# Kernel optimization log

Measured on AMD Instinct MI355X. Metric: run time of the kernel, lower is better.

The kernel has to match this reference:

```python
import jax, jax.numpy as jnp
import numpy as np

N, F, K, E = 65536, 256, 8, 2097152  # nodes, feat dim, experts, edges (avg degree 32)


def setup_inputs() -> dict:
    key = jax.random.key(0)
    ks = jax.random.split(key, 7)
    x = jax.random.normal(ks[0], (N, F), dtype=jnp.float32)
    h0 = jax.random.normal(ks[1], (N, F), dtype=jnp.float32)
    z = jax.random.uniform(ks[2], (N, K), dtype=jnp.float32)
    rows = jax.random.randint(ks[3], (E,), 0, N, dtype=jnp.int32)
    cols = jax.random.randint(ks[4], (E,), 0, N, dtype=jnp.int32)
    # normalized-ish edge weights (like sym-normalized adjacency values)
    vals = jax.random.uniform(ks[5], (E,), dtype=jnp.float32) / 32.0
    stdv = 1.0 / np.sqrt(F)  # reset_parameters: uniform(-stdv, stdv), stdv = 1/sqrt(out)
    weights = jax.random.uniform(ks[6], (K, F, F), minval=-stdv, maxval=stdv, dtype=jnp.float32)
    return {"x": x, "h0": h0, "z": z, "vals": vals, "weights": weights,
            "rows": rows, "cols": cols}


def reference(x, h0, z, vals, weights, rows, cols):
    # hi = spmm(adj, x): irregular gather + segment-sum over edge list
    hi = jax.ops.segment_sum(vals[:, None] * x[cols], rows, num_segments=N)  # [N,F]
    # variant=False: support = hi. Fused K-expert combine:
    # torch: outputs[k] = support @ W[k]; out = sum_k z[:,k,None] * outputs[k]
    out = jnp.einsum('ni,kio,nk->no', hi, weights, z)  # [N,F]
    # residual=True
    return out + x
```

## Files before the change

### kernel.cpp

```cpp
#include <hip/hip_runtime.h>
#include <hip/hip_bf16.h>

using short8 = __attribute__((ext_vector_type(8))) short;
using f32x4  = __attribute__((ext_vector_type(4))) float;
using f32x2  = __attribute__((ext_vector_type(2))) float;
typedef unsigned int u32;

static constexpr int NN = 65536;
static constexpr int F  = 256;
static constexpr int KE = 8;
static constexpr int KD = KE * F;
static constexpr int NB = 256;
static constexpr int EPB = 8192;
static constexpr int BCAP = 12288;

__device__ __forceinline__ short f2bf(float f) {
    union { __hip_bfloat16 h; short s; } u;
    u.h = __float2bfloat16(f);
    return u.s;
}

__device__ __forceinline__ void gld_lds16(void* lds, const void* g) {
    __builtin_amdgcn_global_load_lds((const __attribute__((address_space(1))) u32*)g,
                                     (__attribute__((address_space(3))) u32*)lds, 16, 0, 0);
}

__global__ __launch_bounds__(256)
void conv_x8(const float* __restrict__ x, u32* __restrict__ xq,
             int* __restrict__ bcursor) {
    if (blockIdx.x == 0 && threadIdx.x < NB)
        bcursor[threadIdx.x] = threadIdx.x * BCAP;
    const size_t i = ((size_t)blockIdx.x * 256 + threadIdx.x) * 8;
    const float4 a = *(const float4*)(x + i);
    const float4 b = *(const float4*)(x + i + 4);
    u32 w0 = __builtin_amdgcn_cvt_pk_fp8_f32(a.x, a.y, 0, false);
    w0     = __builtin_amdgcn_cvt_pk_fp8_f32(a.z, a.w, w0, true);
    u32 w1 = __builtin_amdgcn_cvt_pk_fp8_f32(b.x, b.y, 0, false);
    w1     = __builtin_amdgcn_cvt_pk_fp8_f32(b.z, b.w, w1, true);
    *(uint2*)(xq + i / 4) = make_uint2(w0, w1);
}

__global__ void prep_w(const float* __restrict__ W, short* __restrict__ WbT) {
    __shared__ float tile[64][65];
    const int e   = blockIdx.z;
    const int i0b = blockIdx.x;
    const int wc  = blockIdx.y;
    const int c  = threadIdx.x & 63;
    const int r4 = threadIdx.x >> 6;
    for (int rr = r4; rr < 64; rr += 4)
        tile[rr][c] = W[((size_t)e * F + i0b * 64 + rr) * F + wc * 64 + c];
    __syncthreads();
    const int s = e * 4 + i0b;
    #pragma unroll
    for (int q = 0; q < 2; ++q) {
        const int ci   = threadIdx.x + q * 256;
        const int nk   = ci >> 6;
        const int lane = ci & 63;
        const int ni = nk >> 1, ks = nk & 1;
        const int hi2 = lane >> 4, lr = lane & 15;
        const int o_l = ni * 16 + lr;
        const int i_l = ks * 32 + hi2 * 8;
        short8 pk;
        #pragma unroll
        for (int j = 0; j < 8; ++j) pk[j] = f2bf(tile[i_l + j][o_l]);
        *(short8*)(WbT + ((((size_t)(wc * 32 + s) * 8 + nk) << 6) + lane) * 8) = pk;
    }
}

__global__ __launch_bounds__(256)
void bucket_scatter(const int* __restrict__ rows, const int* __restrict__ cols,
                    const float* __restrict__ vals, int* __restrict__ bcursor,
                    int2* __restrict__ tmp, int E) {
    __shared__ int h[NB], wb[NB];
    const int tid = threadIdx.x;
    h[tid] = 0;
    __syncthreads();
    const int base = blockIdx.x * EPB;
    const int lim  = min(EPB, E - base);
    for (int i = tid; i < lim; i += 256)
        atomicAdd(&h[rows[base + i] >> 8], 1);
    __syncthreads();
    const int c = h[tid];
    wb[tid] = c ? atomicAdd(&bcursor[tid], c) : 0;
    h[tid] = 0;
    __syncthreads();
    for (int i = tid; i < lim; i += 256) {
        const int r  = rows[base + i];
        const int bk = r >> 8;
        const int rank = atomicAdd(&h[bk], 1);
        tmp[wb[bk] + rank] = make_int2(((r & 255) << 16) | cols[base + i],
                                       __float_as_int(vals[base + i]));
    }
}

__global__ __launch_bounds__(256)
void bucket_to_csr(const int* __restrict__ bcursor, int2* __restrict__ tmp,
                   int* __restrict__ offsets, int* __restrict__ rend) {
    __shared__ int2 buf[BCAP];
    __shared__ int h[NB], off[NB];
    const int tid = threadIdx.x;
    const int k   = blockIdx.x;
    const int beg = k * BCAP;
    const int n   = bcursor[k] - beg;
    h[tid] = 0;
    __syncthreads();
    for (int i = tid; i < n; i += 256) {
        const int2 e = tmp[beg + i];
        if (i < BCAP) buf[i] = e;
        atomicAdd(&h[e.x >> 16], 1);
    }
    __syncthreads();
    const int c = h[tid];
    off[tid] = c;
    __syncthreads();
    for (int o = 1; o < NB; o <<= 1) {
        int v = (tid >= o) ? off[tid - o] : 0;
        __syncthreads();
        off[tid] += v;
        __syncthreads();
    }
    const int excl = off[tid] - c;
    offsets[k * NB + tid] = beg + excl;
    rend[k * NB + tid]    = beg + excl + c;
    h[tid] = excl;
    __syncthreads();
    for (int i = tid; i < n; i += 256) {
        const int2 e = (i < BCAP) ? buf[i] : tmp[beg + i];
        const int r = e.x >> 16;
        const int pos = atomicAdd(&h[r], 1);
        tmp[beg + pos] = make_int2(e.x & 0xFFFF, e.y);
    }
}

__global__ __launch_bounds__(256)
void gather_rows(const u32* __restrict__ xq, const int2* __restrict__ scv,
                 const int* __restrict__ offsets, const int* __restrict__ rend,
                 float* __restrict__ hi) {
    const int lane = threadIdx.x & 63;
    int row = (blockIdx.x << 2) + (threadIdx.x >> 6);
    row = __builtin_amdgcn_readfirstlane(row);
    const int beg = offsets[row];
    const int end = rend[row];
    float4 acc = {0.f, 0.f, 0.f, 0.f};
    int j = beg;
    for (; j + 8 <= end; j += 8) {
        int2 cc[8];
        u32  rr[8];
        #pragma unroll
        for (int q = 0; q < 8; ++q) cc[q] = scv[j + q];
        #pragma unroll
        for (int q = 0; q < 8; ++q)
            rr[q] = (xq + (size_t)cc[q].x * (F / 4))[lane];
        #pragma unroll
        for (int q = 0; q < 8; ++q) {
            const float v = __int_as_float(cc[q].y);
            const f32x2 lo = __builtin_amdgcn_cvt_pk_f32_fp8(rr[q], false);
            const f32x2 hi2 = __builtin_amdgcn_cvt_pk_f32_fp8(rr[q], true);
            acc.x += v * lo[0];  acc.y += v * lo[1];
            acc.z += v * hi2[0]; acc.w += v * hi2[1];
        }
    }
    for (; j < end; ++j) {
        const int2 c0 = scv[j];
        const u32 r0 = (xq + (size_t)c0.x * (F / 4))[lane];
        const float v0 = __int_as_float(c0.y);
        const f32x2 lo = __builtin_amdgcn_cvt_pk_f32_fp8(r0, false);
        const f32x2 hi2 = __builtin_amdgcn_cvt_pk_f32_fp8(r0, true);
        acc.x += v0 * lo[0];  acc.y += v0 * lo[1];
        acc.z += v0 * hi2[0]; acc.w += v0 * hi2[1];
    }
    ((float4*)(hi + (size_t)row * F))[lane] = acc;
}

#define BM 128
__global__ __launch_bounds__(1024, 4)
void moe_gemm(const float* __restrict__ hi, const float* __restrict__ z,
              const short* __restrict__ WbT, const float* __restrict__ x,
              float* __restrict__ out) {
    __shared__ short A_lds[4][BM * 64];
    __shared__ float z_t[KE][BM];
    const int tid  = threadIdx.x;
    const int lane = tid & 63;
    const int w    = tid >> 6;
    const int wr   = w >> 2;
    const int wc   = w & 3;
    const int row0 = blockIdx.x * BM;

    z_t[tid & 7][tid >> 3] = z[(size_t)row0 * KE + tid];
    {
        const int m0 = tid >> 5;
        const int c8 = tid & 31;
        for (int p = 0; p < BM / 32; ++p) {
            const int m = p * 32 + m0;
            const float4* src = (const float4*)(hi + (size_t)(row0 + m) * F + c8 * 8);
            const float4 a = src[0], b = src[1];
            short8 pk;
            pk[0]=f2bf(a.x); pk[1]=f2bf(a.y); pk[2]=f2bf(a.z); pk[3]=f2bf(a.w);
            pk[4]=f2bf(b.x); pk[5]=f2bf(b.y); pk[6]=f2bf(b.z); pk[7]=f2bf(b.w);
            const int byte = m * 128 + (((c8 & 7) * 16) ^ ((m & 7) << 4));
            *(short8*)((char*)&A_lds[c8 >> 3][0] + byte) = pk;
        }
    }
    __syncthreads();

    f32x4 acc_t[2][4];
    #pragma unroll
    for (int mi = 0; mi < 2; ++mi)
        #pragma unroll
        for (int ni = 0; ni < 4; ++ni)
            acc_t[mi][ni] = (f32x4){0.f, 0.f, 0.f, 0.f};

    const int lr    = lane & 15;
    const int kq16  = (lane >> 4) * 16;
    const int rbase = (lane >> 4) * 4;

    const short* Bw = WbT + ((size_t)wc * 256 << 9) + lane * 8;

    #pragma unroll 1
    for (int s = 0; s < 32; ++s) {
        const int e = s >> 2;

        short8 bf[8];
        const short* ps = Bw + ((size_t)s * 8 << 9);
        #pragma unroll
        for (int nk = 0; nk < 8; ++nk)
            bf[nk] = *(const short8*)(ps + ((size_t)nk << 9));

        #pragma unroll
        for (int mi = 0; mi < 2; ++mi) {
            const int m = wr * 32 + mi * 16 + lr;
            short8 af[2];
            #pragma unroll
            for (int ks = 0; ks < 2; ++ks) {
                const int slot = ks * 64 + kq16;
                af[ks] = *(const short8*)((const char*)&A_lds[s & 3][0]
                            + m * 128 + (slot ^ ((m & 7) << 4)));
            }
            f32x4 pe[4];
            #pragma unroll
            for (int ni = 0; ni < 4; ++ni) pe[ni] = (f32x4){0.f, 0.f, 0.f, 0.f};
            #pragma unroll
            for (int ks = 0; ks < 2; ++ks)
                #pragma unroll
                for (int ni = 0; ni < 4; ++ni)
                    pe[ni] = __builtin_amdgcn_mfma_f32_16x16x32_bf16(
                        af[ks], bf[ni * 2 + ks], pe[ni], 0, 0, 0);
            const f32x4 zv = *(const f32x4*)&z_t[e][wr * 32 + mi * 16 + rbase];
            #pragma unroll
            for (int ni = 0; ni < 4; ++ni)
                #pragma unroll
                for (int r = 0; r < 4; ++r)
                    acc_t[mi][ni][r] += zv[r] * pe[ni][r];
        }
    }

    #pragma unroll
    for (int mi = 0; mi < 2; ++mi) {
        #pragma unroll
        for (int r = 0; r < 4; ++r) {
            const int m = wr * 32 + mi * 16 + rbase + r;
            const size_t rowoff = (size_t)(row0 + m) * F;
            #pragma unroll
            for (int ni = 0; ni < 4; ++ni) {
                const int o = wc * 64 + ni * 16 + lr;
                out[rowoff + o] = acc_t[mi][ni][r] + x[rowoff + o];
            }
        }
    }
}

extern "C" void kernel_launch(void* const* d_in, const int* in_sizes, int n_in,
                              void* d_out, int out_size, void* d_ws, size_t ws_size,
                              hipStream_t stream) {
    const float* x    = (const float*)d_in[0];
    const float* z    = (const float*)d_in[2];
    const float* vals = (const float*)d_in[3];
    const float* W    = (const float*)d_in[4];
    const int* rows   = (const int*)d_in[5];
    const int* cols   = (const int*)d_in[6];
    float* out        = (float*)d_out;
    const int E = in_sizes[3];

    char* ws = (char*)d_ws;
    u32*   xq      = (u32*)  (ws);
    short* WbT     = (short*)(ws + ((size_t)16 << 20));
    int*   offsets = (int*)  (ws + ((size_t)17 << 20));
    int*   rend    = (int*)  (ws + ((size_t)17 << 20) + 256*1024);
    int*   bcursor = (int*)  (ws + ((size_t)17 << 20) + 512*1024);
    int2*  tmp     = (int2*) (ws + ((size_t)18 << 20));
    float* hi      = out;

    const int nblk = (E + EPB - 1) / EPB;
    conv_x8<<<(NN * F) / (256 * 8), 256, 0, stream>>>(x, xq, bcursor);
    prep_w<<<dim3(4, 4, 8), 256, 0, stream>>>(W, WbT);
    bucket_scatter<<<nblk, 256, 0, stream>>>(rows, cols, vals, bcursor, tmp, E);
    bucket_to_csr<<<NB, 256, 0, stream>>>(bcursor, tmp, offsets, rend);
    gather_rows<<<NN / 4, 256, 0, stream>>>(xq, tmp, offsets, rend, hi);
    moe_gemm<<<NN / BM, 1024, 0, stream>>>(hi, z, WbT, x, out);
}
```

Before: 242.5 us.

## Fuse sparse row gather into MoE GEMM prologue, writing bf16 directly to LDS

Result: slower. 259.2 us (+6.9%).

```diff
diff --git a/kernel.cpp b/kernel.cpp
--- a/kernel.cpp
+++ b/kernel.cpp
@@ -18,11 +18,6 @@
     union { __hip_bfloat16 h; short s; } u;
     u.h = __float2bfloat16(f);
     return u.s;
-}
-
-__device__ __forceinline__ void gld_lds16(void* lds, const void* g) {
-    __builtin_amdgcn_global_load_lds((const __attribute__((address_space(1))) u32*)g,
-                                     (__attribute__((address_space(3))) u32*)lds, 16, 0, 0);
 }
 
 __global__ __launch_bounds__(256)
@@ -132,51 +127,12 @@
     }
 }
 
-__global__ __launch_bounds__(256)
-void gather_rows(const u32* __restrict__ xq, const int2* __restrict__ scv,
-                 const int* __restrict__ offsets, const int* __restrict__ rend,
-                 float* __restrict__ hi) {
-    const int lane = threadIdx.x & 63;
-    int row = (blockIdx.x << 2) + (threadIdx.x >> 6);
-    row = __builtin_amdgcn_readfirstlane(row);
-    const int beg = offsets[row];
-    const int end = rend[row];
-    float4 acc = {0.f, 0.f, 0.f, 0.f};
-    int j = beg;
-    for (; j + 8 <= end; j += 8) {
-        int2 cc[8];
-        u32  rr[8];
-        #pragma unroll
-        for (int q = 0; q < 8; ++q) cc[q] = scv[j + q];
-        #pragma unroll
-        for (int q = 0; q < 8; ++q)
-            rr[q] = (xq + (size_t)cc[q].x * (F / 4))[lane];
-        #pragma unroll
-        for (int q = 0; q < 8; ++q) {
-            const float v = __int_as_float(cc[q].y);
-            const f32x2 lo = __builtin_amdgcn_cvt_pk_f32_fp8(rr[q], false);
-            const f32x2 hi2 = __builtin_amdgcn_cvt_pk_f32_fp8(rr[q], true);
-            acc.x += v * lo[0];  acc.y += v * lo[1];
-            acc.z += v * hi2[0]; acc.w += v * hi2[1];
-        }
-    }
-    for (; j < end; ++j) {
-        const int2 c0 = scv[j];
-        const u32 r0 = (xq + (size_t)c0.x * (F / 4))[lane];
-        const float v0 = __int_as_float(c0.y);
-        const f32x2 lo = __builtin_amdgcn_cvt_pk_f32_fp8(r0, false);
-        const f32x2 hi2 = __builtin_amdgcn_cvt_pk_f32_fp8(r0, true);
-        acc.x += v0 * lo[0];  acc.y += v0 * lo[1];
-        acc.z += v0 * hi2[0]; acc.w += v0 * hi2[1];
-    }
-    ((float4*)(hi + (size_t)row * F))[lane] = acc;
-}
-
 #define BM 128
 __global__ __launch_bounds__(1024, 4)
-void moe_gemm(const float* __restrict__ hi, const float* __restrict__ z,
-              const short* __restrict__ WbT, const float* __restrict__ x,
-              float* __restrict__ out) {
+void moe_gemm(const u32* __restrict__ xq, const int2* __restrict__ scv,
+              const int* __restrict__ offsets, const int* __restrict__ rend,
+              const float* __restrict__ z, const short* __restrict__ WbT,
+              const float* __restrict__ x, float* __restrict__ out) {
     __shared__ short A_lds[4][BM * 64];
     __shared__ float z_t[KE][BM];
     const int tid  = threadIdx.x;
@@ -187,18 +143,50 @@
     const int row0 = blockIdx.x * BM;
 
     z_t[tid & 7][tid >> 3] = z[(size_t)row0 * KE + tid];
+
     {
-        const int m0 = tid >> 5;
-        const int c8 = tid & 31;
-        for (int p = 0; p < BM / 32; ++p) {
-            const int m = p * 32 + m0;
-            const float4* src = (const float4*)(hi + (size_t)(row0 + m) * F + c8 * 8);
-            const float4 a = src[0], b = src[1];
-            short8 pk;
-            pk[0]=f2bf(a.x); pk[1]=f2bf(a.y); pk[2]=f2bf(a.z); pk[3]=f2bf(a.w);
-            pk[4]=f2bf(b.x); pk[5]=f2bf(b.y); pk[6]=f2bf(b.z); pk[7]=f2bf(b.w);
-            const int byte = m * 128 + (((c8 & 7) * 16) ^ ((m & 7) << 4));
-            *(short8*)((char*)&A_lds[c8 >> 3][0] + byte) = pk;
+        const int sl    = lane >> 4;
+        const int base8 = (lane & 15) * 8;
+        const int slotx = ((base8 >> 4) * 16);
+        const int sub8  = base8 & 8;
+        for (int ri = 0; ri < 8; ++ri) {
+            const int m   = w * 8 + ri;
+            const int row = row0 + m;
+            const int beg = offsets[row];
+            const int end = rend[row];
+            float4 acc = {0.f, 0.f, 0.f, 0.f};
+            int j = beg;
+            for (; j + 8 <= end; j += 8) {
+                int2 cc[8];
+                u32  rr[8];
+                #pragma unroll
+                for (int q = 0; q < 8; ++q) cc[q] = scv[j + q];
+                #pragma unroll
+                for (int q = 0; q < 8; ++q)
+                    rr[q] = (xq + (size_t)cc[q].x * (F / 4))[lane];
+                #pragma unroll
+                for (int q = 0; q < 8; ++q) {
+                    const float v = __int_as_float(cc[q].y);
+                    const f32x2 lo = __builtin_amdgcn_cvt_pk_f32_fp8(rr[q], false);
+                    const f32x2 hi2 = __builtin_amdgcn_cvt_pk_f32_fp8(rr[q], true);
+                    acc.x += v * lo[0];  acc.y += v * lo[1];
+                    acc.z += v * hi2[0]; acc.w += v * hi2[1];
+                }
+            }
+            for (; j < end; ++j) {
+                const int2 c0 = scv[j];
+                const u32 r0 = (xq + (size_t)c0.x * (F / 4))[lane];
+                const float v0 = __int_as_float(c0.y);
+                const f32x2 lo = __builtin_amdgcn_cvt_pk_f32_fp8(r0, false);
+                const f32x2 hi2 = __builtin_amdgcn_cvt_pk_f32_fp8(r0, true);
+                acc.x += v0 * lo[0];  acc.y += v0 * lo[1];
+                acc.z += v0 * hi2[0]; acc.w += v0 * hi2[1];
+            }
+            union { short s[4]; int2 i2; } o;
+            o.s[0] = f2bf(acc.x); o.s[1] = f2bf(acc.y);
+            o.s[2] = f2bf(acc.z); o.s[3] = f2bf(acc.w);
+            const int byte = m * 128 + (slotx ^ ((m & 7) << 4)) + sub8;
+            *(int2*)((char*)&A_lds[sl][0] + byte) = o.i2;
         }
     }
     __syncthreads();
@@ -288,13 +276,11 @@
     int*   rend    = (int*)  (ws + ((size_t)17 << 20) + 256*1024);
     int*   bcursor = (int*)  (ws + ((size_t)17 << 20) + 512*1024);
     int2*  tmp     = (int2*) (ws + ((size_t)18 << 20));
-    float* hi      = out;
 
     const int nblk = (E + EPB - 1) / EPB;
     conv_x8<<<(NN * F) / (256 * 8), 256, 0, stream>>>(x, xq, bcursor);
     prep_w<<<dim3(4, 4, 8), 256, 0, stream>>>(W, WbT);
     bucket_scatter<<<nblk, 256, 0, stream>>>(rows, cols, vals, bcursor, tmp, E);
     bucket_to_csr<<<NB, 256, 0, stream>>>(bcursor, tmp, offsets, rend);
-    gather_rows<<<NN / 4, 256, 0, stream>>>(xq, tmp, offsets, rend, hi);
-    moe_gemm<<<NN / BM, 1024, 0, stream>>>(hi, z, WbT, x, out);
-}
+    moe_gemm<<<NN / BM, 1024, 0, stream>>>(xq, tmp, offsets, rend, z, WbT, x, out);
+}
```
